# Kernel tuning notes

Measured on AMD Instinct MI355X. Metric: run time of the kernel, lower is better.

## Reference

```python
import jax, jax.numpy as jnp
import numpy as np

B, T, C = 32, 1024, 512
D = C // 2          # reduction_factor_input = 2 -> conv1d(1x1) filters = 256
U = 256             # LSTM units
O = U // 1          # reduction_factor_output = 1 -> 256


def setup_inputs() -> dict:
    key = jax.random.key(0)
    ks = jax.random.split(key, 8)
    s = lambda *d: 1.0 / np.sqrt(d[0])
    return {
        "x": jax.random.normal(ks[0], (B, T, C), jnp.float32),
        "w_in": jax.random.normal(ks[1], (C, D), jnp.float32) * s(C),
        "b_in": jnp.zeros((D,), jnp.float32),
        "kernel": jax.random.normal(ks[2], (D, 4 * U), jnp.float32) * s(D),
        "rec_kernel": jax.random.normal(ks[3], (U, 4 * U), jnp.float32) * s(U),
        "bias": jnp.zeros((4 * U,), jnp.float32),
        "w_out": jax.random.normal(ks[4], (U, O), jnp.float32) * s(U),
        "b_out": jnp.zeros((O,), jnp.float32),
    }


def _lstm(xz, rec_kernel):
    # xz: [T, B, 4U] precomputed input projection (x @ kernel + bias)
    def step(carry, xt):
        h, c = carry
        z = xt + h @ rec_kernel  # [B, 4U]
        i, f, g, o = jnp.split(z, 4, axis=-1)  # Keras gate order: i, f, c, o
        i = jax.nn.sigmoid(i)
        f = jax.nn.sigmoid(f)
        g = jnp.tanh(g)
        o = jax.nn.sigmoid(o)
        c = f * c + i * g
        h = o * jnp.tanh(c)
        return (h, c), h

    b = xz.shape[1]
    init = (jnp.zeros((b, U), xz.dtype), jnp.zeros((b, U), xz.dtype))
    _, hs = jax.lax.scan(step, init, xz)
    return hs  # [T, B, U]


def reference(x, w_in, b_in, kernel, rec_kernel, bias, w_out, b_out):
    # Conv1D kernel_size=1 == per-timestep dense projection
    xin = x @ w_in + b_in                      # [B, T, D]
    xz = xin @ kernel + bias                   # [B, T, 4U]
    hs = _lstm(jnp.transpose(xz, (1, 0, 2)), rec_kernel)  # [T, B, U]
    hs = jnp.transpose(hs, (1, 0, 2))          # [B, T, U]
    return hs @ w_out + b_out                  # [B, T, O]
```

## Files before the change

kernel.cpp:

```cpp
#include <hip/hip_runtime.h>


#define DEV static __device__ __forceinline__

typedef __attribute__((ext_vector_type(8))) short short8;
typedef __attribute__((ext_vector_type(4))) float floatx4;
typedef _Float16 half2v __attribute__((ext_vector_type(2)));

static constexpr int Bsz = 32, T = 1024, C = 512, D = 256, U = 256, FU = 1024;
static constexpr int M = Bsz * T;

DEV float bfu2f(unsigned int u) { union { unsigned int i; float f; } v; v.i = u; return v.f; }
DEV float bf2f(unsigned short u) { return bfu2f(((unsigned int)u) << 16); }
DEV unsigned short f2bf(float f) {
    union { float f; unsigned int i; } v; v.f = f;
    return (unsigned short)((v.i + 0x7fffu + ((v.i >> 16) & 1u)) >> 16);
}
DEV float sigmf(float x) { return 1.0f / (1.0f + __expf(-x)); }
DEV float tanhfast(float x) {
    const float a = __expf(-2.0f * fabsf(x));
    const float t = (1.0f - a) / (1.0f + a);
    return copysignf(t, x);
}

DEV float dot2h(unsigned int w, unsigned int a, float acc) {
#if __has_builtin(__builtin_amdgcn_fdot2)
    return __builtin_amdgcn_fdot2(__builtin_bit_cast(half2v, w),
                                  __builtin_bit_cast(half2v, a), acc, false);
#else
    const half2v wv = __builtin_bit_cast(half2v, w);
    const half2v av = __builtin_bit_cast(half2v, a);
    return acc + (float)wv[0] * (float)av[0] + (float)wv[1] * (float)av[1];
#endif
}

DEV short ld_bf(const float* p) { return (short)f2bf(*p); }
DEV short ld_bf(const unsigned short* p) { return (short)*p; }
DEV short8 ld_frag(const unsigned short* p) { return *(const short8*)p; }
DEV short8 ld_frag(const float* p) {
    short8 v;
#pragma unroll
    for (int j = 0; j < 8; j++) v[j] = (short)f2bf(p[j]);
    return v;
}
DEV float ldxz1(const float* p) { return *p; }
DEV float ldxz1(const unsigned short* p) { return bf2f(*p); }

template <int K, int N, int MT, int NS, bool OUTF32, typename AT, typename BT>
__global__ __launch_bounds__(64) void gemm_mfma(
    const AT* __restrict__ A,
    const BT* __restrict__ Bm,
    const float* __restrict__ bias,
    void* __restrict__ Cv)
{
    constexpr int KC = K / 32;
    const int lane = threadIdx.x;
    const int quad = lane >> 4, lr = lane & 15;
    constexpr int NSG = N / (16 * NS);
    const int sg = blockIdx.x % NSG;
    const int mb = blockIdx.x / NSG;
    const int n0 = sg * 16 * NS;

    short8 bf[NS][KC];
    float biasv[NS];
#pragma unroll
    for (int s = 0; s < NS; s++) {
        const int n = n0 + s * 16 + lr;
        biasv[s] = bias[n];
#pragma unroll
        for (int kc = 0; kc < KC; kc++) {
            short8 v;
#pragma unroll
            for (int j = 0; j < 8; j++) {
                const int k = kc * 32 + quad * 8 + j;
                v[j] = ld_bf(&Bm[(size_t)k * N + n]);
            }
            bf[s][kc] = v;
        }
    }

    for (int mt = 0; mt < MT; mt++) {
        const int m0 = (mb * MT + mt) * 16;
        const AT* Ap = A + (size_t)(m0 + lr) * K + quad * 8;
        floatx4 acc[NS];
#pragma unroll
        for (int s = 0; s < NS; s++) acc[s] = (floatx4){0.f, 0.f, 0.f, 0.f};
#pragma unroll
        for (int kc = 0; kc < KC; kc++) {
            short8 af = ld_frag(Ap + kc * 32);
#pragma unroll
            for (int s = 0; s < NS; s++)
                acc[s] = __builtin_amdgcn_mfma_f32_16x16x32_bf16(af, bf[s][kc], acc[s], 0, 0, 0);
        }
#pragma unroll
        for (int s = 0; s < NS; s++) {
            const int n = n0 + s * 16 + lr;
#pragma unroll
            for (int r = 0; r < 4; r++) {
                const int m = m0 + quad * 4 + r;
                const float val = acc[s][r] + biasv[s];
                if (OUTF32)
                    ((float*)Cv)[(size_t)m * N + n] = val;
                else
                    ((unsigned short*)Cv)[(size_t)m * N + n] = f2bf(val);
            }
        }
    }
}

__global__ __launch_bounds__(256) void pack_rec(const float* __restrict__ rec,
                                                uint4* __restrict__ P)
{
    const int i = blockIdx.x * 256 + threadIdx.x;
    const int g = i >> 10, c = i & 1023;
    uint4 v;
    unsigned int* vp = (unsigned int*)&v;
#pragma unroll
    for (int r = 0; r < 4; r++) {
        const _Float16 lo = (_Float16)rec[(size_t)(8 * g + 2 * r) * FU + c];
        const _Float16 hi = (_Float16)rec[(size_t)(8 * g + 2 * r + 1) * FU + c];
        vp[r] = (unsigned int)__builtin_bit_cast(unsigned short, lo)
              | ((unsigned int)__builtin_bit_cast(unsigned short, hi) << 16);
    }
    P[i] = v;
}

template <typename XZT>
__global__ __attribute__((amdgpu_flat_work_group_size(512, 512),
                          amdgpu_waves_per_eu(2, 2)))
void lstm_kernel(
    const XZT* __restrict__ xz,
    const uint4* __restrict__ P,
    unsigned short* __restrict__ hs)
{
    const int b = blockIdx.x;
    const int tid = threadIdx.x;
    const int lane = tid & 63;
    const int c0 = tid;
    const int c1 = tid + 512;

    __shared__ uint4 Wl[8 * 1024];
    __shared__ float z_sh[FU];
    __shared__ unsigned short h_pk[U];

#pragma unroll
    for (int g = 0; g < 8; g++) {
        Wl[g * 1024 + c0] = P[(size_t)(24 + g) * 1024 + c0];
        Wl[g * 1024 + c1] = P[(size_t)(24 + g) * 1024 + c1];
    }
    float cst = 0.f;
    if (tid < U) h_pk[tid] = 0;

    uint4 w0[24], w1[24];
#pragma unroll
    for (int g = 0; g < 24; g++) {
        w0[g] = P[(size_t)g * 1024 + c0];
        w1[g] = P[(size_t)g * 1024 + c1];
    }
#pragma unroll
    for (int g = 0; g < 24; g++) {
        asm volatile("" : "+v"(w0[g].x), "+v"(w0[g].y), "+v"(w0[g].z), "+v"(w0[g].w));
        asm volatile("" : "+v"(w1[g].x), "+v"(w1[g].y), "+v"(w1[g].z), "+v"(w1[g].w));
    }
    __syncthreads();

    const XZT* xzb = xz + (size_t)b * T * FU;
    unsigned short* hsb = hs + (size_t)b * T * U;

    float xz0n = ldxz1(xzb + c0);
    float xz1n = ldxz1(xzb + c1);

#define RL(kk) ((unsigned int)__builtin_amdgcn_readlane( \
        (int)(((kk) & 1) ? hp.y : hp.x), (kk) >> 1))

    for (int t = 0; t < T; t++) {
        uint4 La[4], Lb[4];
#pragma unroll
        for (int s = 0; s < 4; s++) {
            La[s] = Wl[s * 1024 + c0];
            Lb[s] = Wl[s * 1024 + c1];
        }

        float z0 = xz0n, z1 = xz1n;
        if (t + 1 < T) {
            xz0n = ldxz1(xzb + (size_t)(t + 1) * FU + c0);
            xz1n = ldxz1(xzb + (size_t)(t + 1) * FU + c1);
        }

        const uint2 hp = *(const uint2*)&h_pk[lane * 4];

#pragma unroll
        for (int blk = 0; blk < 8; blk++) {
#pragma unroll
            for (int g = 3 * blk; g < 3 * blk + 3; g++) {
#pragma unroll
                for (int r = 0; r < 4; r++) {
                    const unsigned int a_ = RL(4 * g + r);
                    z0 = dot2h(w0[g][r], a_, z0);
                    z1 = dot2h(w1[g][r], a_, z1);
                }
            }
            {
                const uint4 wa = La[blk & 3], wb = Lb[blk & 3];
#pragma unroll
                for (int r = 0; r < 4; r++) {
                    const unsigned int a_ = RL(96 + 4 * blk + r);
                    z0 = dot2h(wa[r], a_, z0);
                    z1 = dot2h(wb[r], a_, z1);
                }
                if (blk < 4) {
                    La[blk & 3] = Wl[(blk + 4) * 1024 + c0];
                    Lb[blk & 3] = Wl[(blk + 4) * 1024 + c1];
                }
            }
        }

        z_sh[c0] = z0;
        z_sh[c1] = z1;
        __syncthreads();
        if (tid < U) {
            const float iv = sigmf(z_sh[tid]);
            const float fv = sigmf(z_sh[tid + U]);
            const float gv = tanhfast(z_sh[tid + 2 * U]);
            const float ov = sigmf(z_sh[tid + 3 * U]);
            cst = fv * cst + iv * gv;
            const float hv = ov * tanhfast(cst);
            h_pk[tid] = __builtin_bit_cast(unsigned short, (_Float16)hv);
            hsb[(size_t)t * U + tid] = f2bf(hv);
        }
        __syncthreads();
    }
#undef RL
}

extern "C" void kernel_launch(void* const* d_in, const int* in_sizes, int n_in,
                              void* d_out, int out_size, void* d_ws, size_t ws_size,
                              hipStream_t stream)
{
    const float* x    = (const float*)d_in[0];
    const float* w_in = (const float*)d_in[1];
    const float* b_in = (const float*)d_in[2];
    const float* kern = (const float*)d_in[3];
    const float* rec  = (const float*)d_in[4];
    const float* bias = (const float*)d_in[5];
    const float* wout = (const float*)d_in[6];
    const float* bout = (const float*)d_in[7];

    char* ws = (char*)d_ws;
    const size_t rec_bytes = (size_t)32 * 1024 * 16;
    const size_t xin_bytes = (size_t)M * D * 2;
    const size_t hs_bytes  = (size_t)M * U * 2;
    const size_t xz32_bytes = (size_t)M * FU * 4;
    const size_t base = rec_bytes + xin_bytes + hs_bytes;

    uint4* P = (uint4*)ws;
    unsigned short* xin_bf = (unsigned short*)(ws + rec_bytes);
    unsigned short* hs_bf  = (unsigned short*)(ws + rec_bytes + xin_bytes);
    char* xz_raw = ws + base;

    const bool use_f32 = ws_size >= base + xz32_bytes;

    pack_rec<<<(32 * 1024) / 256, 256, 0, stream>>>(rec, P);

    gemm_mfma<512, 256, 16, 2, false><<<(256 / 32) * (M / 256), 64, 0, stream>>>(
        x, w_in, b_in, (void*)xin_bf);

    if (use_f32) {
        float* xz = (float*)xz_raw;
        gemm_mfma<256, 1024, 16, 2, true><<<(1024 / 32) * (M / 256), 64, 0, stream>>>(
            xin_bf, kern, bias, (void*)xz);
        lstm_kernel<float><<<Bsz, 512, 0, stream>>>(xz, P, hs_bf);
    } else {
        unsigned short* xz = (unsigned short*)xz_raw;
        gemm_mfma<256, 1024, 16, 2, false><<<(1024 / 32) * (M / 256), 64, 0, stream>>>(
            xin_bf, kern, bias, (void*)xz);
        lstm_kernel<unsigned short><<<Bsz, 512, 0, stream>>>(xz, P, hs_bf);
    }

    gemm_mfma<256, 256, 16, 2, true><<<(256 / 32) * (M / 256), 64, 0, stream>>>(
        hs_bf, wout, bout, d_out);
}
```

Baseline: 2.316 ms.

## Compute LSTM recurrent matvec with fp16 MFMA instead of fdot2 readlane loops

Replaces the per-thread fdot2 recurrent matvec, which broadcasts h with readlane, with 16x16x32 f16 MFMA instructions. h is fed as the A operand with only one active row (lr==0), and the recurrent weights are repacked into MFMA fragment layout, split between registers and LDS. Each wave computes gates for its own 32 hidden units, so the z_sh staging pass is gone. h is double-buffered, leaving one barrier per timestep instead of two. In exchange, 15 of the 16 MFMA rows do no useful work, so the dependent chain of MFMA latency per step could dominate.

Result: faster. 2.156 ms (-6.9%).

```diff
diff --git a/kernel.cpp b/kernel.cpp
--- a/kernel.cpp
+++ b/kernel.cpp
@@ -5,7 +5,7 @@
 
 typedef __attribute__((ext_vector_type(8))) short short8;
 typedef __attribute__((ext_vector_type(4))) float floatx4;
-typedef _Float16 half2v __attribute__((ext_vector_type(2)));
+typedef _Float16 half8 __attribute__((ext_vector_type(8)));
 
 static constexpr int Bsz = 32, T = 1024, C = 512, D = 256, U = 256, FU = 1024;
 static constexpr int M = Bsz * T;
@@ -22,17 +22,7 @@
     const float t = (1.0f - a) / (1.0f + a);
     return copysignf(t, x);
 }
-
-DEV float dot2h(unsigned int w, unsigned int a, float acc) {
-#if __has_builtin(__builtin_amdgcn_fdot2)
-    return __builtin_amdgcn_fdot2(__builtin_bit_cast(half2v, w),
-                                  __builtin_bit_cast(half2v, a), acc, false);
-#else
-    const half2v wv = __builtin_bit_cast(half2v, w);
-    const half2v av = __builtin_bit_cast(half2v, a);
-    return acc + (float)wv[0] * (float)av[0] + (float)wv[1] * (float)av[1];
-#endif
-}
+DEV half8 h8c(uint4 v) { return __builtin_bit_cast(half8, v); }
 
 DEV short ld_bf(const float* p) { return (short)f2bf(*p); }
 DEV short ld_bf(const unsigned short* p) { return (short)*p; }
@@ -108,129 +98,160 @@
     }
 }
 
-__global__ __launch_bounds__(256) void pack_rec(const float* __restrict__ rec,
-                                                uint4* __restrict__ P)
+__global__ __launch_bounds__(256) void pack_rec_mfma(const float* __restrict__ rec,
+                                                     uint4* __restrict__ Pm)
 {
-    const int i = blockIdx.x * 256 + threadIdx.x;
-    const int g = i >> 10, c = i & 1023;
-    uint4 v;
-    unsigned int* vp = (unsigned int*)&v;
-#pragma unroll
-    for (int r = 0; r < 4; r++) {
-        const _Float16 lo = (_Float16)rec[(size_t)(8 * g + 2 * r) * FU + c];
-        const _Float16 hi = (_Float16)rec[(size_t)(8 * g + 2 * r + 1) * FU + c];
-        vp[r] = (unsigned int)__builtin_bit_cast(unsigned short, lo)
-              | ((unsigned int)__builtin_bit_cast(unsigned short, hi) << 16);
-    }
-    P[i] = v;
+    const int idx = blockIdx.x * 256 + threadIdx.x;
+    const int lane = idx & 63;
+    const int kc = (idx >> 6) & 7;
+    const int strip = idx >> 9;
+    const int q = lane >> 4, lr = lane & 15;
+    const int col = strip * 16 + lr;
+    const int k0 = kc * 32 + q * 8;
+    union { unsigned short u[8]; uint4 v; } out;
+#pragma unroll
+    for (int j = 0; j < 8; j++) {
+        const _Float16 h = (_Float16)rec[(size_t)(k0 + j) * FU + col];
+        out.u[j] = __builtin_bit_cast(unsigned short, h);
+    }
+    Pm[idx] = out.v;
 }
 
 template <typename XZT>
 __global__ __attribute__((amdgpu_flat_work_group_size(512, 512),
                           amdgpu_waves_per_eu(2, 2)))
-void lstm_kernel(
+void lstm_mfma(
     const XZT* __restrict__ xz,
-    const uint4* __restrict__ P,
+    const uint4* __restrict__ Pm,
     unsigned short* __restrict__ hs)
 {
     const int b = blockIdx.x;
     const int tid = threadIdx.x;
+    const int w = tid >> 6;
     const int lane = tid & 63;
-    const int c0 = tid;
-    const int c1 = tid + 512;
-
-    __shared__ uint4 Wl[8 * 1024];
-    __shared__ float z_sh[FU];
-    __shared__ unsigned short h_pk[U];
-
-#pragma unroll
-    for (int g = 0; g < 8; g++) {
-        Wl[g * 1024 + c0] = P[(size_t)(24 + g) * 1024 + c0];
-        Wl[g * 1024 + c1] = P[(size_t)(24 + g) * 1024 + c1];
-    }
-    float cst = 0.f;
-    if (tid < U) h_pk[tid] = 0;
-
-    uint4 w0[24], w1[24];
-#pragma unroll
-    for (int g = 0; g < 24; g++) {
-        w0[g] = P[(size_t)g * 1024 + c0];
-        w1[g] = P[(size_t)g * 1024 + c1];
-    }
-#pragma unroll
-    for (int g = 0; g < 24; g++) {
-        asm volatile("" : "+v"(w0[g].x), "+v"(w0[g].y), "+v"(w0[g].z), "+v"(w0[g].w));
-        asm volatile("" : "+v"(w1[g].x), "+v"(w1[g].y), "+v"(w1[g].z), "+v"(w1[g].w));
-    }
+    const int q = lane >> 4, lr = lane & 15;
+
+    __shared__ uint4 Wl[16 * 8 * 64];
+    __shared__ __align__(16) unsigned short hbuf[2][U];
+
+    for (int i = tid; i < 16 * 8 * 64; i += 512)
+        Wl[i] = Pm[48 * 8 * 64 + i];
+    if (tid < U) { hbuf[0][tid] = 0; hbuf[1][tid] = 0; }
+
+    uint4 Wr[6][8];
+#pragma unroll
+    for (int s = 0; s < 6; s++) {
+        const int strip = (s >> 1) * 16 + 2 * w + (s & 1);
+#pragma unroll
+        for (int kc = 0; kc < 8; kc++)
+            Wr[s][kc] = Pm[(strip * 8 + kc) * 64 + lane];
+    }
+#pragma unroll
+    for (int s = 0; s < 6; s++)
+#pragma unroll
+        for (int kc = 0; kc < 8; kc++)
+            asm volatile("" : "+v"(Wr[s][kc].x), "+v"(Wr[s][kc].y),
+                             "+v"(Wr[s][kc].z), "+v"(Wr[s][kc].w));
     __syncthreads();
 
     const XZT* xzb = xz + (size_t)b * T * FU;
     unsigned short* hsb = hs + (size_t)b * T * U;
-
-    float xz0n = ldxz1(xzb + c0);
-    float xz1n = ldxz1(xzb + c1);
-
-#define RL(kk) ((unsigned int)__builtin_amdgcn_readlane( \
-        (int)(((kk) & 1) ? hp.y : hp.x), (kk) >> 1))
+    const int u0 = 32 * w + lr;
+
+    float c0 = 0.f, c1 = 0.f;
+    float xc[8], xn[8];
+#pragma unroll
+    for (int i = 0; i < 8; i++) { xc[i] = 0.f; xn[i] = 0.f; }
+    if (q == 0) {
+#pragma unroll
+        for (int g2 = 0; g2 < 4; g2++) {
+            xc[2 * g2]     = ldxz1(xzb + g2 * 256 + u0);
+            xc[2 * g2 + 1] = ldxz1(xzb + g2 * 256 + u0 + 16);
+        }
+    }
+
+    const uint4 z4 = {0u, 0u, 0u, 0u};
+    uint4 afc = z4, afn = z4;
 
     for (int t = 0; t < T; t++) {
-        uint4 La[4], Lb[4];
-#pragma unroll
-        for (int s = 0; s < 4; s++) {
-            La[s] = Wl[s * 1024 + c0];
-            Lb[s] = Wl[s * 1024 + c1];
-        }
-
-        float z0 = xz0n, z1 = xz1n;
-        if (t + 1 < T) {
-            xz0n = ldxz1(xzb + (size_t)(t + 1) * FU + c0);
-            xz1n = ldxz1(xzb + (size_t)(t + 1) * FU + c1);
-        }
-
-        const uint2 hp = *(const uint2*)&h_pk[lane * 4];
-
-#pragma unroll
-        for (int blk = 0; blk < 8; blk++) {
-#pragma unroll
-            for (int g = 3 * blk; g < 3 * blk + 3; g++) {
-#pragma unroll
-                for (int r = 0; r < 4; r++) {
-                    const unsigned int a_ = RL(4 * g + r);
-                    z0 = dot2h(w0[g][r], a_, z0);
-                    z1 = dot2h(w1[g][r], a_, z1);
+        const unsigned short* hb = hbuf[t & 1];
+        unsigned short* hn = hbuf[(t + 1) & 1];
+
+        const XZT* xzt1 = xzb + (size_t)(t + 1 < T ? t + 1 : t) * FU;
+        if (q == 0) {
+#pragma unroll
+            for (int g2 = 0; g2 < 4; g2++) {
+                xn[2 * g2]     = ldxz1(xzt1 + g2 * 256 + u0);
+                xn[2 * g2 + 1] = ldxz1(xzt1 + g2 * 256 + u0 + 16);
+            }
+        }
+
+        {
+            floatx4 acc_i = {0.f,0.f,0.f,0.f}, acc_f = {0.f,0.f,0.f,0.f};
+            floatx4 acc_g = {0.f,0.f,0.f,0.f}, acc_o = {0.f,0.f,0.f,0.f};
+            if (lr == 0) afc = *(const uint4*)(hb + q * 8);
+            uint4 stc = Wl[(2 * w * 8) * 64 + lane], stn = z4;
+#pragma unroll
+            for (int kc = 0; kc < 8; kc++) {
+                if (kc < 7) {
+                    if (lr == 0) afn = *(const uint4*)(hb + (kc + 1) * 32 + q * 8);
+                    stn = Wl[(2 * w * 8 + kc + 1) * 64 + lane];
                 }
-            }
-            {
-                const uint4 wa = La[blk & 3], wb = Lb[blk & 3];
-#pragma unroll
-                for (int r = 0; r < 4; r++) {
-                    const unsigned int a_ = RL(96 + 4 * blk + r);
-                    z0 = dot2h(wa[r], a_, z0);
-                    z1 = dot2h(wb[r], a_, z1);
+                acc_i = __builtin_amdgcn_mfma_f32_16x16x32_f16(h8c(afc), h8c(Wr[0][kc]), acc_i, 0, 0, 0);
+                acc_f = __builtin_amdgcn_mfma_f32_16x16x32_f16(h8c(afc), h8c(Wr[2][kc]), acc_f, 0, 0, 0);
+                acc_g = __builtin_amdgcn_mfma_f32_16x16x32_f16(h8c(afc), h8c(Wr[4][kc]), acc_g, 0, 0, 0);
+                acc_o = __builtin_amdgcn_mfma_f32_16x16x32_f16(h8c(afc), h8c(stc),       acc_o, 0, 0, 0);
+                afc = afn; stc = stn;
+            }
+            const float zi = acc_i[0] + xc[0];
+            const float zf = acc_f[0] + xc[2];
+            const float zg = acc_g[0] + xc[4];
+            const float zo = acc_o[0] + xc[6];
+            const float iv = sigmf(zi), fv = sigmf(zf);
+            const float gv = tanhfast(zg), ov = sigmf(zo);
+            c0 = fv * c0 + iv * gv;
+            const float hv = ov * tanhfast(c0);
+            if (q == 0) {
+                hn[u0] = __builtin_bit_cast(unsigned short, (_Float16)hv);
+                hsb[(size_t)t * U + u0] = f2bf(hv);
+            }
+        }
+
+        {
+            floatx4 acc_i = {0.f,0.f,0.f,0.f}, acc_f = {0.f,0.f,0.f,0.f};
+            floatx4 acc_g = {0.f,0.f,0.f,0.f}, acc_o = {0.f,0.f,0.f,0.f};
+            if (lr == 0) afc = *(const uint4*)(hb + q * 8);
+            uint4 stc = Wl[((2 * w + 1) * 8) * 64 + lane], stn = z4;
+#pragma unroll
+            for (int kc = 0; kc < 8; kc++) {
+                if (kc < 7) {
+                    if (lr == 0) afn = *(const uint4*)(hb + (kc + 1) * 32 + q * 8);
+                    stn = Wl[((2 * w + 1) * 8 + kc + 1) * 64 + lane];
                 }
-                if (blk < 4) {
-                    La[blk & 3] = Wl[(blk + 4) * 1024 + c0];
-                    Lb[blk & 3] = Wl[(blk + 4) * 1024 + c1];
-                }
-            }
-        }
-
-        z_sh[c0] = z0;
-        z_sh[c1] = z1;
+                acc_i = __builtin_amdgcn_mfma_f32_16x16x32_f16(h8c(afc), h8c(Wr[1][kc]), acc_i, 0, 0, 0);
+                acc_f = __builtin_amdgcn_mfma_f32_16x16x32_f16(h8c(afc), h8c(Wr[3][kc]), acc_f, 0, 0, 0);
+                acc_g = __builtin_amdgcn_mfma_f32_16x16x32_f16(h8c(afc), h8c(Wr[5][kc]), acc_g, 0, 0, 0);
+                acc_o = __builtin_amdgcn_mfma_f32_16x16x32_f16(h8c(afc), h8c(stc),       acc_o, 0, 0, 0);
+                afc = afn; stc = stn;
+            }
+            const float zi = acc_i[0] + xc[1];
+            const float zf = acc_f[0] + xc[3];
+            const float zg = acc_g[0] + xc[5];
+            const float zo = acc_o[0] + xc[7];
+            const float iv = sigmf(zi), fv = sigmf(zf);
+            const float gv = tanhfast(zg), ov = sigmf(zo);
+            c1 = fv * c1 + iv * gv;
+            const float hv = ov * tanhfast(c1);
+            if (q == 0) {
+                hn[u0 + 16] = __builtin_bit_cast(unsigned short, (_Float16)hv);
+                hsb[(size_t)t * U + u0 + 16] = f2bf(hv);
+            }
+        }
+
+#pragma unroll
+        for (int i = 0; i < 8; i++) xc[i] = xn[i];
         __syncthreads();
-        if (tid < U) {
-            const float iv = sigmf(z_sh[tid]);
-            const float fv = sigmf(z_sh[tid + U]);
-            const float gv = tanhfast(z_sh[tid + 2 * U]);
-            const float ov = sigmf(z_sh[tid + 3 * U]);
-            cst = fv * cst + iv * gv;
-            const float hv = ov * tanhfast(cst);
-            h_pk[tid] = __builtin_bit_cast(unsigned short, (_Float16)hv);
-            hsb[(size_t)t * U + tid] = f2bf(hv);
-        }
-        __syncthreads();
-    }
-#undef RL
+    }
 }
 
 extern "C" void kernel_launch(void* const* d_in, const int* in_sizes, int n_in,
@@ -247,7 +268,7 @@
     const float* bout = (const float*)d_in[7];
 
     char* ws = (char*)d_ws;
-    const size_t rec_bytes = (size_t)32 * 1024 * 16;
+    const size_t rec_bytes = (size_t)64 * 8 * 64 * 16;
     const size_t xin_bytes = (size_t)M * D * 2;
     const size_t hs_bytes  = (size_t)M * U * 2;
     const size_t xz32_bytes = (size_t)M * FU * 4;
@@ -260,7 +281,7 @@
 
     const bool use_f32 = ws_size >= base + xz32_bytes;
 
-    pack_rec<<<(32 * 1024) / 256, 256, 0, stream>>>(rec, P);
+    pack_rec_mfma<<<128, 256, 0, stream>>>(rec, P);
 
     gemm_mfma<512, 256, 16, 2, false><<<(256 / 32) * (M / 256), 64, 0, stream>>>(
         x, w_in, b_in, (void*)xin_bf);
@@ -269,12 +290,12 @@
         float* xz = (float*)xz_raw;
         gemm_mfma<256, 1024, 16, 2, true><<<(1024 / 32) * (M / 256), 64, 0, stream>>>(
             xin_bf, kern, bias, (void*)xz);
-        lstm_kernel<float><<<Bsz, 512, 0, stream>>>(xz, P, hs_bf);
+        lstm_mfma<float><<<Bsz, 512, 0, stream>>>(xz, P, hs_bf);
     } else {
         unsigned short* xz = (unsigned short*)xz_raw;
         gemm_mfma<256, 1024, 16, 2, false><<<(1024 / 32) * (M / 256), 64, 0, stream>>>(
             xin_bf, kern, bias, (void*)xz);
-        lstm_kernel<unsigned short><<<Bsz, 512, 0, stream>>>(xz, P, hs_bf);
+        lstm_mfma<unsigned short><<<Bsz, 512, 0, stream>>>(xz, P, hs_bf);
     }
 
     gemm_mfma<256, 256, 16, 2, true><<<(256 / 32) * (M / 256), 64, 0, stream>>>(
```

## Use packed fp16 FMA for LSTM recurrence with LDS-broadcast hidden state

Applied to the files above, without the earlier changes.

Replaces the fdot2/readlane recurrent matvec with v_pk_fma_f16, where each thread packs two gate columns (c and c+512) into one half2 accumulator. The hidden state is read as uint4 broadcasts from double-buffered LDS instead of readlane. Gate activations for f/o are computed in the upper half of the block and shared through LDS, and the barriers become a lighter waitcnt+s_barrier. This cuts instruction count per step, but accumulating in fp16 risks precision loss over 256-term sums.

New measurement: 2.373 ms. 1.02x slower.

```diff
diff --git a/kernel.cpp b/kernel.cpp
--- a/kernel.cpp
+++ b/kernel.cpp
@@ -23,17 +23,6 @@
     return copysignf(t, x);
 }
 
-DEV float dot2h(unsigned int w, unsigned int a, float acc) {
-#if __has_builtin(__builtin_amdgcn_fdot2)
-    return __builtin_amdgcn_fdot2(__builtin_bit_cast(half2v, w),
-                                  __builtin_bit_cast(half2v, a), acc, false);
-#else
-    const half2v wv = __builtin_bit_cast(half2v, w);
-    const half2v av = __builtin_bit_cast(half2v, a);
-    return acc + (float)wv[0] * (float)av[0] + (float)wv[1] * (float)av[1];
-#endif
-}
-
 DEV short ld_bf(const float* p) { return (short)f2bf(*p); }
 DEV short ld_bf(const unsigned short* p) { return (short)*p; }
 DEV short8 ld_frag(const unsigned short* p) { return *(const short8*)p; }
@@ -45,6 +34,15 @@
 }
 DEV float ldxz1(const float* p) { return *p; }
 DEV float ldxz1(const unsigned short* p) { return bf2f(*p); }
+
+#define PK_LO(acc, w, h) \
+    asm("v_pk_fma_f16 %0, %1, %2, %0 op_sel:[0,0,0] op_sel_hi:[1,0,1]" \
+        : "+v"(acc) : "v"(w), "v"(h))
+#define PK_HI(acc, w, h) \
+    asm("v_pk_fma_f16 %0, %1, %2, %0 op_sel:[0,1,0] op_sel_hi:[1,1,1]" \
+        : "+v"(acc) : "v"(w), "v"(h))
+
+#define BAR() asm volatile("s_waitcnt lgkmcnt(0)\n\ts_barrier" ::: "memory")
 
 template <int K, int N, int MT, int NS, bool OUTF32, typename AT, typename BT>
 __global__ __launch_bounds__(64) void gemm_mfma(
@@ -108,129 +106,120 @@
     }
 }
 
-__global__ __launch_bounds__(256) void pack_rec(const float* __restrict__ rec,
-                                                uint4* __restrict__ P)
-{
-    const int i = blockIdx.x * 256 + threadIdx.x;
-    const int g = i >> 10, c = i & 1023;
-    uint4 v;
-    unsigned int* vp = (unsigned int*)&v;
-#pragma unroll
-    for (int r = 0; r < 4; r++) {
-        const _Float16 lo = (_Float16)rec[(size_t)(8 * g + 2 * r) * FU + c];
-        const _Float16 hi = (_Float16)rec[(size_t)(8 * g + 2 * r + 1) * FU + c];
-        vp[r] = (unsigned int)__builtin_bit_cast(unsigned short, lo)
-              | ((unsigned int)__builtin_bit_cast(unsigned short, hi) << 16);
-    }
-    P[i] = v;
+__global__ __launch_bounds__(256) void pack_rec_pk(const float* __restrict__ rec,
+                                                   unsigned int* __restrict__ Pres,
+                                                   unsigned int* __restrict__ Pst)
+{
+    const int idx = blockIdx.x * 256 + threadIdx.x;
+    const int k = idx >> 9, c = idx & 511;
+    const _Float16 lo = (_Float16)rec[(size_t)k * FU + c];
+    const _Float16 hi = (_Float16)rec[(size_t)k * FU + c + 512];
+    const unsigned int v = (unsigned int)__builtin_bit_cast(unsigned short, lo)
+                         | ((unsigned int)__builtin_bit_cast(unsigned short, hi) << 16);
+    const int s = k >> 5, e8 = k & 7, b3 = (k >> 3) & 3;
+    if (b3 < 3)
+        Pres[(size_t)(s * 24 + b3 * 8 + e8) * 512 + c] = v;
+    else
+        Pst[((size_t)(s * 2 + (e8 >> 2)) * 512 + c) * 4 + (e8 & 3)] = v;
 }
 
 template <typename XZT>
 __global__ __attribute__((amdgpu_flat_work_group_size(512, 512),
                           amdgpu_waves_per_eu(2, 2)))
-void lstm_kernel(
+void lstm_pk(
     const XZT* __restrict__ xz,
-    const uint4* __restrict__ P,
+    const unsigned int* __restrict__ Pres,
+    const uint4* __restrict__ Pst,
     unsigned short* __restrict__ hs)
 {
     const int b = blockIdx.x;
     const int tid = threadIdx.x;
-    const int lane = tid & 63;
-    const int c0 = tid;
-    const int c1 = tid + 512;
-
-    __shared__ uint4 Wl[8 * 1024];
-    __shared__ float z_sh[FU];
-    __shared__ unsigned short h_pk[U];
-
-#pragma unroll
-    for (int g = 0; g < 8; g++) {
-        Wl[g * 1024 + c0] = P[(size_t)(24 + g) * 1024 + c0];
-        Wl[g * 1024 + c1] = P[(size_t)(24 + g) * 1024 + c1];
-    }
-    float cst = 0.f;
-    if (tid < U) h_pk[tid] = 0;
-
-    uint4 w0[24], w1[24];
-#pragma unroll
-    for (int g = 0; g < 24; g++) {
-        w0[g] = P[(size_t)g * 1024 + c0];
-        w1[g] = P[(size_t)g * 1024 + c1];
-    }
-#pragma unroll
-    for (int g = 0; g < 24; g++) {
-        asm volatile("" : "+v"(w0[g].x), "+v"(w0[g].y), "+v"(w0[g].z), "+v"(w0[g].w));
-        asm volatile("" : "+v"(w1[g].x), "+v"(w1[g].y), "+v"(w1[g].z), "+v"(w1[g].w));
-    }
+
+    __shared__ uint4 Ws[16 * 512];
+    __shared__ float2 zsh[U];
+    __shared__ __align__(16) unsigned short hpk[2][U];
+
+#pragma unroll
+    for (int j = 0; j < 16; j++) Ws[j * 512 + tid] = Pst[j * 512 + tid];
+    if (tid < U) { hpk[0][tid] = 0; hpk[1][tid] = 0; }
+
+    unsigned int Wr[192];
+#pragma unroll
+    for (int i = 0; i < 192; i++) Wr[i] = Pres[(size_t)i * 512 + tid];
+#pragma unroll
+    for (int i = 0; i < 192; i++) asm volatile("" : "+v"(Wr[i]));
     __syncthreads();
 
     const XZT* xzb = xz + (size_t)b * T * FU;
     unsigned short* hsb = hs + (size_t)b * T * U;
 
-    float xz0n = ldxz1(xzb + c0);
-    float xz1n = ldxz1(xzb + c1);
-
-#define RL(kk) ((unsigned int)__builtin_amdgcn_readlane( \
-        (int)(((kk) & 1) ? hp.y : hp.x), (kk) >> 1))
+    float cst = 0.f;
+    float xz0 = ldxz1(xzb + tid);
+    float xz1 = ldxz1(xzb + tid + 512);
 
     for (int t = 0; t < T; t++) {
-        uint4 La[4], Lb[4];
-#pragma unroll
-        for (int s = 0; s < 4; s++) {
-            La[s] = Wl[s * 1024 + c0];
-            Lb[s] = Wl[s * 1024 + c1];
-        }
-
-        float z0 = xz0n, z1 = xz1n;
+        float xz0n = 0.f, xz1n = 0.f;
         if (t + 1 < T) {
-            xz0n = ldxz1(xzb + (size_t)(t + 1) * FU + c0);
-            xz1n = ldxz1(xzb + (size_t)(t + 1) * FU + c1);
-        }
-
-        const uint2 hp = *(const uint2*)&h_pk[lane * 4];
-
-#pragma unroll
-        for (int blk = 0; blk < 8; blk++) {
-#pragma unroll
-            for (int g = 3 * blk; g < 3 * blk + 3; g++) {
-#pragma unroll
-                for (int r = 0; r < 4; r++) {
-                    const unsigned int a_ = RL(4 * g + r);
-                    z0 = dot2h(w0[g][r], a_, z0);
-                    z1 = dot2h(w1[g][r], a_, z1);
+            xz0n = ldxz1(xzb + (size_t)(t + 1) * FU + tid);
+            xz1n = ldxz1(xzb + (size_t)(t + 1) * FU + tid + 512);
+        }
+
+        const uint4* HP = (const uint4*)hpk[t & 1];
+        unsigned int a0 = 0, a1 = 0, a2 = 0, a3 = 0;
+
+        uint4 L[4];
+        L[0] = Ws[0 * 512 + tid]; L[1] = Ws[1 * 512 + tid];
+        L[2] = Ws[2 * 512 + tid]; L[3] = Ws[3 * 512 + tid];
+
+#pragma unroll
+        for (int sb = 0; sb < 8; sb++) {
+#pragma unroll
+            for (int bb = 0; bb < 3; bb++) {
+                const uint4 hb = HP[sb * 4 + bb];
+                const int w0 = sb * 24 + bb * 8;
+                PK_LO(a0, Wr[w0 + 0], hb.x); PK_HI(a1, Wr[w0 + 1], hb.x);
+                PK_LO(a2, Wr[w0 + 2], hb.y); PK_HI(a3, Wr[w0 + 3], hb.y);
+                PK_LO(a0, Wr[w0 + 4], hb.z); PK_HI(a1, Wr[w0 + 5], hb.z);
+                PK_LO(a2, Wr[w0 + 6], hb.w); PK_HI(a3, Wr[w0 + 7], hb.w);
+            }
+            {
+                const uint4 hb = HP[sb * 4 + 3];
+                const uint4 wa = L[(sb & 1) * 2], wb = L[(sb & 1) * 2 + 1];
+                PK_LO(a0, wa.x, hb.x); PK_HI(a1, wa.y, hb.x);
+                PK_LO(a2, wa.z, hb.y); PK_HI(a3, wa.w, hb.y);
+                PK_LO(a0, wb.x, hb.z); PK_HI(a1, wb.y, hb.z);
+                PK_LO(a2, wb.z, hb.w); PK_HI(a3, wb.w, hb.w);
+                if (sb < 6) {
+                    L[(sb & 1) * 2]     = Ws[((sb + 2) * 2 + 0) * 512 + tid];
+                    L[(sb & 1) * 2 + 1] = Ws[((sb + 2) * 2 + 1) * 512 + tid];
                 }
             }
-            {
-                const uint4 wa = La[blk & 3], wb = Lb[blk & 3];
-#pragma unroll
-                for (int r = 0; r < 4; r++) {
-                    const unsigned int a_ = RL(96 + 4 * blk + r);
-                    z0 = dot2h(wa[r], a_, z0);
-                    z1 = dot2h(wb[r], a_, z1);
-                }
-                if (blk < 4) {
-                    La[blk & 3] = Wl[(blk + 4) * 1024 + c0];
-                    Lb[blk & 3] = Wl[(blk + 4) * 1024 + c1];
-                }
-            }
-        }
-
-        z_sh[c0] = z0;
-        z_sh[c1] = z1;
-        __syncthreads();
+        }
+
+        float z0 = xz0, z1 = xz1;
+        {
+            half2v p;
+            p = __builtin_bit_cast(half2v, a0); z0 += (float)p[0]; z1 += (float)p[1];
+            p = __builtin_bit_cast(half2v, a1); z0 += (float)p[0]; z1 += (float)p[1];
+            p = __builtin_bit_cast(half2v, a2); z0 += (float)p[0]; z1 += (float)p[1];
+            p = __builtin_bit_cast(half2v, a3); z0 += (float)p[0]; z1 += (float)p[1];
+        }
+
+        if (tid >= U) zsh[tid - U] = make_float2(sigmf(z0), sigmf(z1));
+        BAR();
         if (tid < U) {
-            const float iv = sigmf(z_sh[tid]);
-            const float fv = sigmf(z_sh[tid + U]);
-            const float gv = tanhfast(z_sh[tid + 2 * U]);
-            const float ov = sigmf(z_sh[tid + 3 * U]);
-            cst = fv * cst + iv * gv;
-            const float hv = ov * tanhfast(cst);
-            h_pk[tid] = __builtin_bit_cast(unsigned short, (_Float16)hv);
+            const float2 fo = zsh[tid];
+            const float iv = sigmf(z0);
+            const float gv = tanhfast(z1);
+            cst = fo.x * cst + iv * gv;
+            const float hv = fo.y * tanhfast(cst);
+            hpk[(t + 1) & 1][tid] = __builtin_bit_cast(unsigned short, (_Float16)hv);
             hsb[(size_t)t * U + tid] = f2bf(hv);
         }
-        __syncthreads();
-    }
-#undef RL
+        BAR();
+
+        xz0 = xz0n; xz1 = xz1n;
+    }
 }
 
 extern "C" void kernel_launch(void* const* d_in, const int* in_sizes, int n_in,
@@ -247,34 +236,35 @@
     const float* bout = (const float*)d_in[7];
 
     char* ws = (char*)d_ws;
-    const size_t rec_bytes = (size_t)32 * 1024 * 16;
+    const size_t rec_bytes = (size_t)512 * 1024;
     const size_t xin_bytes = (size_t)M * D * 2;
     const size_t hs_bytes  = (size_t)M * U * 2;
     const size_t xz32_bytes = (size_t)M * FU * 4;
     const size_t base = rec_bytes + xin_bytes + hs_bytes;
 
-    uint4* P = (uint4*)ws;
+    unsigned int* Pres = (unsigned int*)ws;
+    unsigned int* Pst  = (unsigned int*)(ws + (size_t)384 * 1024);
     unsigned short* xin_bf = (unsigned short*)(ws + rec_bytes);
     unsigned short* hs_bf  = (unsigned short*)(ws + rec_bytes + xin_bytes);
     char* xz_raw = ws + base;
 
     const bool use_f32 = ws_size >= base + xz32_bytes;
 
-    pack_rec<<<(32 * 1024) / 256, 256, 0, stream>>>(rec, P);
+    pack_rec_pk<<<512, 256, 0, stream>>>(rec, Pres, Pst);
 
     gemm_mfma<512, 256, 16, 2, false><<<(256 / 32) * (M / 256), 64, 0, stream>>>(
         x, w_in, b_in, (void*)xin_bf);
 
     if (use_f32) {
-        float* xz = (float*)xz_raw;
+        float* xzp = (float*)xz_raw;
         gemm_mfma<256, 1024, 16, 2, true><<<(1024 / 32) * (M / 256), 64, 0, stream>>>(
-            xin_bf, kern, bias, (void*)xz);
-        lstm_kernel<float><<<Bsz, 512, 0, stream>>>(xz, P, hs_bf);
+            xin_bf, kern, bias, (void*)xzp);
+        lstm_pk<float><<<Bsz, 512, 0, stream>>>(xzp, Pres, (const uint4*)Pst, hs_bf);
     } else {
-        unsigned short* xz = (unsigned short*)xz_raw;
+        unsigned short* xzp = (unsigned short*)xz_raw;
         gemm_mfma<256, 1024, 16, 2, false><<<(1024 / 32) * (M / 256), 64, 0, stream>>>(
-            xin_bf, kern, bias, (void*)xz);
-        lstm_kernel<unsigned short><<<Bsz, 512, 0, stream>>>(xz, P, hs_bf);
+            xin_bf, kern, bias, (void*)xzp);
+        lstm_pk<unsigned short><<<Bsz, 512, 0, stream>>>(xzp, Pres, (const uint4*)Pst, hs_bf);
     }
 
     gemm_mfma<256, 256, 16, 2, true><<<(256 / 32) * (M / 256), 64, 0, stream>>>(
```
